# Optimization experiments

Measured on AMD Instinct MI355X. Metric: run time of the kernel, lower is better.

## Reference

```python
import jax, jax.numpy as jnp
import numpy as np

B, L, HID, NH = 4, 1024, 768, 12
HD = HID // NH  # head dim 64
VOCAB, MPE = 30, 2048
NW, WL = 8, 16
BETA = 1.0


def setup_inputs() -> dict:
    key = jax.random.key(0)
    ks = jax.random.split(key, 10)
    hidden_states = jax.random.normal(ks[0], (B, L, HID), dtype=jnp.float32)
    attention_mask = jnp.zeros((B, 1, 1, L), dtype=jnp.float32)
    distance = jax.random.randint(ks[1], (B, L, L), 0, 1022, dtype=jnp.int32)
    random_walk = jax.random.randint(ks[2], (B, L, NW, WL), 0, VOCAB, dtype=jnp.int32)
    anonymous_random_walk = jax.random.randint(ks[3], (B, L, NW, WL), 0, VOCAB, dtype=jnp.int32)
    s = 0.02
    Wq = jax.random.normal(ks[4], (HID, HID), dtype=jnp.float32) * s
    Wk = jax.random.normal(ks[5], (HID, HID), dtype=jnp.float32) * s
    Wv = jax.random.normal(ks[6], (HID, HID), dtype=jnp.float32) * s
    bq = jnp.zeros((HID,), jnp.float32)
    bk = jnp.zeros((HID,), jnp.float32)
    bv = jnp.zeros((HID,), jnp.float32)
    node_emb = jax.random.normal(ks[7], (VOCAB, HID), dtype=jnp.float32) * s
    node_emb = node_emb.at[0].set(0.0)  # padding_idx=0
    dist_emb = jax.random.normal(ks[8], (MPE, NH), dtype=jnp.float32) * s
    dist_emb = dist_emb.at[0].set(0.0)  # padding_idx=0
    return dict(hidden_states=hidden_states, attention_mask=attention_mask,
                Wq=Wq, bq=bq, Wk=Wk, bk=bk, Wv=Wv, bv=bv,
                node_emb=node_emb, dist_emb=dist_emb,
                distance=distance, random_walk=random_walk,
                anonymous_random_walk=anonymous_random_walk)


def _heads(x):  # [B,L,HID] -> [B,NH,L,HD]
    return x.reshape(B, L, NH, HD).transpose(0, 2, 1, 3)


def _walk_bias(walk, node_emb):
    # walk: [B,L,NW,WL] int -> embed [B,L,NW,WL,HID] -> sum dims (2,3) -> [B,L,HID]
    pe = jnp.sum(node_emb[walk], axis=(2, 3))
    e = _heads(pe)  # [B,NH,L,HD]
    return jnp.einsum('bhid,bhjd->bhij', e, e)


def reference(hidden_states, attention_mask, Wq, bq, Wk, bk, Wv, bv,
              node_emb, dist_emb, distance, random_walk, anonymous_random_walk):
    q = _heads(hidden_states @ Wq.T + bq)
    k = _heads(hidden_states @ Wk.T + bk)
    v = _heads(hidden_states @ Wv.T + bv)
    scores = jnp.einsum('bhid,bhjd->bhij', q, k) / np.sqrt(HD).astype(np.float32)
    # distance RPE: [B,L,L,NH] -> [B,NH,L,L]
    bias = dist_emb[distance + 1].transpose(0, 3, 1, 2)
    bias = bias + _walk_bias(random_walk, node_emb)
    bias = bias + _walk_bias(anonymous_random_walk, node_emb)
    scores = scores + bias * BETA + attention_mask
    probs = jax.nn.softmax(scores, axis=-1)
    ctx = jnp.einsum('bhij,bhjd->bhid', probs, v)
    return ctx.transpose(0, 2, 1, 3).reshape(B, L, HID)
```

## Files before the change

kernel.cpp:

```cpp
#include <hip/hip_runtime.h>
#include <hip/hip_bf16.h>

#define LL 1024
#define HID 768
#define NH 12
#define HD 64
#define KAUG 192
#define NBH 48

typedef unsigned int u32;
typedef unsigned short u16;
typedef __bf16 bf16_t;
typedef bf16_t bf16x8 __attribute__((ext_vector_type(8)));
typedef float f32x4 __attribute__((ext_vector_type(4)));
typedef u32 u32x4 __attribute__((ext_vector_type(4)));

__device__ __forceinline__ u16 f2b(float f) {
    union { float f; u32 u; } v; v.f = f;
    u32 r = v.u + 0x7fffu + ((v.u >> 16) & 1u);
    return (u16)(r >> 16);
}
__device__ __forceinline__ bf16x8 load8s(const u16* p) {
    return __builtin_bit_cast(bf16x8, *reinterpret_cast<const u32x4*>(p));
}
__device__ __forceinline__ void cvt4_store_v(u16* dst, float4 f) {
    ushort4 o;
    o.x = f2b(f.x); o.y = f2b(f.y); o.z = f2b(f.z); o.w = f2b(f.w);
    *reinterpret_cast<ushort4*>(dst) = o;
}

__global__ __launch_bounds__(256) void k_cvt(const float* __restrict__ hs,
                                             const float* __restrict__ Wq,
                                             const float* __restrict__ Wk,
                                             const float* __restrict__ Wv,
                                             u16* __restrict__ hs_b, u16* __restrict__ Wq_b,
                                             u16* __restrict__ Wk_b, u16* __restrict__ Wv_b) {
    int seg = blockIdx.y;
    const float* src = (seg == 0) ? hs : (seg == 1) ? Wq : (seg == 2) ? Wk : Wv;
    u16* dst         = (seg == 0) ? hs_b : (seg == 1) ? Wq_b : (seg == 2) ? Wk_b : Wv_b;
    int nchunk = (seg == 0) ? 786432 : 147456;
    int c = blockIdx.x * 256 + threadIdx.x;
    if (c >= nchunk) return;
    float4 f = *reinterpret_cast<const float4*>(&src[(size_t)c * 4]);
    cvt4_store_v(&dst[(size_t)c * 4], f);
}

__global__ __launch_bounds__(256) void k_qkv(const u16* __restrict__ hs_b,
                                             const u16* __restrict__ Wq_b, const u16* __restrict__ Wk_b,
                                             const u16* __restrict__ Wv_b,
                                             const float* __restrict__ bq, const float* __restrict__ bk,
                                             const float* __restrict__ bv,
                                             u16* __restrict__ Qa, u16* __restrict__ Ka,
                                             u16* __restrict__ Vt) {
    __shared__ __align__(16) u16 smem[18432];
    u16* a_s = smem;
    u16* b_s = smem + 9216;
    int m0 = blockIdx.x * 128;
    int nt = blockIdx.y;
    int which = nt / 6;
    int n0w = (nt % 6) * 128;
    const u16* W      = (which == 0) ? Wq_b : (which == 1) ? Wk_b : Wv_b;
    const float* bias = (which == 0) ? bq : (which == 1) ? bk : bv;
    int tid = threadIdx.x;
    int wave = tid >> 6, lane = tid & 63, l15 = lane & 15, qd = lane >> 4;
    int wm = wave >> 1, wn = wave & 1;

    f32x4 acc[4][4];
    for (int i = 0; i < 4; i++)
        for (int j = 0; j < 4; j++) acc[i][j] = f32x4{0.f, 0.f, 0.f, 0.f};

    u32x4 pa[4], pb[4];
#pragma unroll
    for (int it = 0; it < 4; it++) {
        int c = tid + it * 256;
        int row = c >> 3, col = (c & 7) * 8;
        pa[it] = *reinterpret_cast<const u32x4*>(&hs_b[(size_t)(m0 + row) * 768 + col]);
        pb[it] = *reinterpret_cast<const u32x4*>(&W[(size_t)(n0w + row) * 768 + col]);
    }
    for (int k0 = 0; k0 < 768; k0 += 64) {
        __syncthreads();
#pragma unroll
        for (int it = 0; it < 4; it++) {
            int c = tid + it * 256;
            int row = c >> 3, col = (c & 7) * 8;
            *reinterpret_cast<u32x4*>(&a_s[row * 72 + col]) = pa[it];
            *reinterpret_cast<u32x4*>(&b_s[row * 72 + col]) = pb[it];
        }
        __syncthreads();
        if (k0 < 704) {
            int k1 = k0 + 64;
#pragma unroll
            for (int it = 0; it < 4; it++) {
                int c = tid + it * 256;
                int row = c >> 3, col = (c & 7) * 8;
                pa[it] = *reinterpret_cast<const u32x4*>(&hs_b[(size_t)(m0 + row) * 768 + k1 + col]);
                pb[it] = *reinterpret_cast<const u32x4*>(&W[(size_t)(n0w + row) * 768 + k1 + col]);
            }
        }
        for (int kk = 0; kk < 2; kk++) {
            bf16x8 af[4], bf[4];
            for (int i = 0; i < 4; i++) af[i] = load8s(&a_s[(wm * 64 + i * 16 + l15) * 72 + kk * 32 + qd * 8]);
            for (int j = 0; j < 4; j++) bf[j] = load8s(&b_s[(wn * 64 + j * 16 + l15) * 72 + kk * 32 + qd * 8]);
            for (int i = 0; i < 4; i++)
                for (int j = 0; j < 4; j++)
                    acc[i][j] = __builtin_amdgcn_mfma_f32_16x16x32_bf16(af[i], bf[j], acc[i][j], 0, 0, 0);
        }
    }
    __syncthreads();
    int b = m0 >> 10, l0b = m0 & 1023;
    if (which != 2) {
        float qscale = (which == 0) ? 0.125f : 1.0f;
        for (int i = 0; i < 4; i++) {
            int m_loc = wm * 64 + i * 16 + qd * 4;
            for (int j = 0; j < 4; j++) {
                int n_loc = wn * 64 + j * 16 + l15;
                float bv_ = bias[n0w + n_loc];
                for (int r = 0; r < 4; r++)
                    smem[(m_loc + r) * 136 + n_loc] = f2b((acc[i][j][r] + bv_) * qscale);
            }
        }
        __syncthreads();
        u16* dstbuf = (which == 0) ? Qa : Ka;
        for (int it = 0; it < 8; it++) {
            int c = tid + it * 256;
            int row = c >> 4, col = (c & 15) * 8;
            u32x4 w = *reinterpret_cast<u32x4*>(&smem[row * 136 + col]);
            int nn = n0w + col;
            int h = nn >> 6, d = nn & 63;
            size_t dst = ((size_t)(b * NH + h) * LL + (l0b + row)) * KAUG + d;
            *reinterpret_cast<u32x4*>(&dstbuf[dst]) = w;
        }
    } else {
        for (int i = 0; i < 4; i++) {
            int m_loc = wm * 64 + i * 16 + qd * 4;
            for (int j = 0; j < 4; j++) {
                int n_loc = wn * 64 + j * 16 + l15;
                float bv_ = bias[n0w + n_loc];
                for (int r = 0; r < 4; r++)
                    smem[n_loc * 136 + (m_loc + r)] = f2b(acc[i][j][r] + bv_);
            }
        }
        __syncthreads();
        for (int it = 0; it < 8; it++) {
            int c = tid + it * 256;
            int n = c >> 4, m_off = (c & 15) * 8;
            u32x4 w = *reinterpret_cast<u32x4*>(&smem[n * 136 + m_off]);
            int nn = n0w + n;
            int h = nn >> 6, d = nn & 63;
            size_t dst = ((size_t)(b * NH + h) * HD + d) * LL + (l0b + m_off);
            *reinterpret_cast<u32x4*>(&Vt[dst]) = w;
        }
    }
}

__global__ __launch_bounds__(256) void k_pe(const int* __restrict__ rw,
                                            const int* __restrict__ arw,
                                            const float* __restrict__ node_emb,
                                            u16* __restrict__ Qa, u16* __restrict__ Ka) {
    int m = blockIdx.x;
    __shared__ int hist[64];
    __shared__ float c1[32], c2[32];
    int t = threadIdx.x;
    if (t < 64) hist[t] = 0;
    __syncthreads();
    if (t < 128) atomicAdd(&hist[rw[m * 128 + t] & 31], 1);
    else         atomicAdd(&hist[32 + (arw[m * 128 + (t - 128)] & 31)], 1);
    __syncthreads();
    if (t < 64) {
        if (t < 32) c1[t] = (float)hist[t];
        else        c2[t - 32] = (float)hist[t];
    }
    __syncthreads();
    int b = m >> 10, l = m & 1023;
    for (int c = t; c < 768; c += 256) {
        float s1 = 0.f, s2 = 0.f;
        for (int v = 0; v < 30; v++) {
            float ne = node_emb[v * 768 + c];
            s1 += c1[v] * ne;
            s2 += c2[v] * ne;
        }
        int h = c >> 6, d = c & 63;
        size_t base = ((size_t)(b * NH + h) * LL + l) * KAUG;
        u16 e1 = f2b(s1), e2 = f2b(s2);
        Qa[base + 64 + d] = e1;  Ka[base + 64 + d] = e1;
        Qa[base + 128 + d] = e2; Ka[base + 128 + d] = e2;
    }
}

__global__ __launch_bounds__(256) void k_attn(const u16* __restrict__ Qa, const u16* __restrict__ Ka,
                                              const u16* __restrict__ Vt,
                                              const int* __restrict__ distance,
                                              const float* __restrict__ dist_emb,
                                              const float* __restrict__ mask,
                                              void* __restrict__ outv, int f32mode) {
    __shared__ __align__(16) u16 ka_s[64][200];
    __shared__ __align__(16) u16 vt_s[64][72];
    __shared__ __align__(16) u16 p_s[4][16][72];

    int itile = blockIdx.x;
    int bh = blockIdx.y;
    int b = bh / NH, h = bh % NH;
    int tid = threadIdx.x, wave = tid >> 6, lane = tid & 63, l15 = lane & 15, qd = lane >> 4;

    const u16* Qh = Qa + (size_t)bh * LL * KAUG;
    const u16* Kh = Ka + (size_t)bh * LL * KAUG;
    const u16* Vh = Vt + (size_t)bh * HD * LL;
    const int* distb = distance + (size_t)b * LL * LL;
    const float* maskb = mask + (size_t)b * LL;
    const float* debh = dist_emb + h;

    int i0 = itile * 64 + wave * 16;
    bf16x8 aq[6];
    for (int ks = 0; ks < 6; ks++)
        aq[ks] = load8s(&Qh[(size_t)(i0 + l15) * KAUG + ks * 32 + qd * 8]);

    f32x4 o[4];
    for (int i = 0; i < 4; i++) o[i] = f32x4{0.f, 0.f, 0.f, 0.f};
    float m_i[4], l_i[4];
    for (int r = 0; r < 4; r++) { m_i[r] = -1e30f; l_i[r] = 0.f; }

    u32x4 kbuf[6], vbuf[2];
#pragma unroll
    for (int it = 0; it < 6; it++) {
        int c = tid + it * 256;
        int row = c / 24, col = (c % 24) * 8;
        kbuf[it] = *reinterpret_cast<const u32x4*>(&Kh[(size_t)row * KAUG + col]);
    }
#pragma unroll
    for (int it = 0; it < 2; it++) {
        int c = tid + it * 256;
        int d = c >> 3, col = (c & 7) * 8;
        vbuf[it] = *reinterpret_cast<const u32x4*>(&Vh[(size_t)d * LL + col]);
    }
    int dpre[16]; float mpre[4];
    for (int nf = 0; nf < 4; nf++) {
        int j_abs = nf * 16 + l15;
        mpre[nf] = maskb[j_abs];
        for (int r = 0; r < 4; r++)
            dpre[nf * 4 + r] = distb[(size_t)(i0 + qd * 4 + r) * LL + j_abs];
    }

    for (int jt = 0; jt < 16; jt++) {
        int j0 = jt * 64;
        __syncthreads();
#pragma unroll
        for (int it = 0; it < 6; it++) {
            int c = tid + it * 256;
            int row = c / 24, col = (c % 24) * 8;
            *reinterpret_cast<u32x4*>(&ka_s[row][col]) = kbuf[it];
        }
#pragma unroll
        for (int it = 0; it < 2; it++) {
            int c = tid + it * 256;
            int d = c >> 3, col = (c & 7) * 8;
            *reinterpret_cast<u32x4*>(&vt_s[d][col]) = vbuf[it];
        }
        __syncthreads();
        int dcur[16]; float mcur[4];
        for (int u_ = 0; u_ < 16; u_++) dcur[u_] = dpre[u_];
        for (int u_ = 0; u_ < 4; u_++)  mcur[u_] = mpre[u_];
        float bias_cur[16];
#pragma unroll
        for (int u_ = 0; u_ < 16; u_++)
            bias_cur[u_] = debh[(size_t)(dcur[u_] + 1) * NH];
        if (jt < 15) {
            int j0n = j0 + 64;
#pragma unroll
            for (int it = 0; it < 6; it++) {
                int c = tid + it * 256;
                int row = c / 24, col = (c % 24) * 8;
                kbuf[it] = *reinterpret_cast<const u32x4*>(&Kh[(size_t)(j0n + row) * KAUG + col]);
            }
#pragma unroll
            for (int it = 0; it < 2; it++) {
                int c = tid + it * 256;
                int d = c >> 3, col = (c & 7) * 8;
                vbuf[it] = *reinterpret_cast<const u32x4*>(&Vh[(size_t)d * LL + j0n + col]);
            }
            for (int nf = 0; nf < 4; nf++) {
                int j_abs = j0n + nf * 16 + l15;
                mpre[nf] = maskb[j_abs];
                for (int r = 0; r < 4; r++)
                    dpre[nf * 4 + r] = distb[(size_t)(i0 + qd * 4 + r) * LL + j_abs];
            }
        }

        f32x4 s[4];
        for (int nf = 0; nf < 4; nf++) {
            f32x4 accv = f32x4{0.f, 0.f, 0.f, 0.f};
            for (int ks = 0; ks < 6; ks++) {
                bf16x8 bfrag = load8s(&ka_s[nf * 16 + l15][ks * 32 + qd * 8]);
                accv = __builtin_amdgcn_mfma_f32_16x16x32_bf16(aq[ks], bfrag, accv, 0, 0, 0);
            }
            s[nf] = accv;
        }
        for (int nf = 0; nf < 4; nf++)
            for (int r = 0; r < 4; r++)
                s[nf][r] += bias_cur[nf * 4 + r] + mcur[nf];
        float mx[4];
        for (int r = 0; r < 4; r++) {
            float v = fmaxf(fmaxf(s[0][r], s[1][r]), fmaxf(s[2][r], s[3][r]));
            for (int off = 1; off < 16; off <<= 1) v = fmaxf(v, __shfl_xor(v, off));
            mx[r] = v;
        }
        float alpha[4], rs[4];
        for (int r = 0; r < 4; r++) {
            float mnew = fmaxf(m_i[r], mx[r]);
            alpha[r] = __expf(m_i[r] - mnew);
            m_i[r] = mnew;
            rs[r] = 0.f;
        }
        for (int nf = 0; nf < 4; nf++)
            for (int r = 0; r < 4; r++) {
                float p = __expf(s[nf][r] - m_i[r]);
                rs[r] += p;
                p_s[wave][qd * 4 + r][nf * 16 + l15] = f2b(p);
            }
        for (int r = 0; r < 4; r++) {
            float v = rs[r];
            for (int off = 1; off < 16; off <<= 1) v += __shfl_xor(v, off);
            l_i[r] = l_i[r] * alpha[r] + v;
        }
        for (int df = 0; df < 4; df++)
            for (int r = 0; r < 4; r++) o[df][r] *= alpha[r];
        __builtin_amdgcn_sched_barrier(0);
        asm volatile("" ::: "memory");
        for (int kstep = 0; kstep < 2; kstep++) {
            bf16x8 ap = load8s(&p_s[wave][l15][kstep * 32 + qd * 8]);
            for (int df = 0; df < 4; df++) {
                bf16x8 bv_ = load8s(&vt_s[df * 16 + l15][kstep * 32 + qd * 8]);
                o[df] = __builtin_amdgcn_mfma_f32_16x16x32_bf16(ap, bv_, o[df], 0, 0, 0);
            }
        }
    }
    for (int df = 0; df < 4; df++) {
        int d = df * 16 + l15;
        for (int r = 0; r < 4; r++) {
            int i_abs = i0 + qd * 4 + r;
            float v = o[df][r] / l_i[r];
            size_t idx = ((size_t)(b * LL) + i_abs) * HID + h * 64 + d;
            if (f32mode) ((float*)outv)[idx] = v;
            else         ((u16*)outv)[idx] = f2b(v);
        }
    }
}

extern "C" void kernel_launch(void* const* d_in, const int* in_sizes, int n_in,
                              void* d_out, int out_size, void* d_ws, size_t ws_size,
                              hipStream_t stream) {
    const float* hs       = (const float*)d_in[0];
    const float* mask     = (const float*)d_in[1];
    const float* Wq       = (const float*)d_in[2];
    const float* bq       = (const float*)d_in[3];
    const float* Wk       = (const float*)d_in[4];
    const float* bk       = (const float*)d_in[5];
    const float* Wv       = (const float*)d_in[6];
    const float* bv       = (const float*)d_in[7];
    const float* node_emb = (const float*)d_in[8];
    const float* dist_emb = (const float*)d_in[9];
    const int* distance   = (const int*)d_in[10];
    const int* rw         = (const int*)d_in[11];
    const int* arw        = (const int*)d_in[12];

    int f32mode = 0;
    {
        hipDeviceptr_t base = nullptr; size_t sz = 0;
        if (hipMemGetAddressRange(&base, &sz, (hipDeviceptr_t)d_out) == hipSuccess) {
            size_t off = (size_t)((char*)d_out - (char*)base);
            if (sz - off >= (size_t)out_size * 4u) f32mode = 1;
        }
    }

    u16* Qa   = (u16*)d_ws;
    u16* Ka   = Qa + (size_t)NBH * LL * KAUG;
    u16* Vt   = Ka + (size_t)NBH * LL * KAUG;
    u16* hs_b = Vt + (size_t)NBH * HD * LL;
    u16* Wq_b = hs_b + (size_t)4096 * 768;
    u16* Wk_b = Wq_b + (size_t)768 * 768;
    u16* Wv_b = Wk_b + (size_t)768 * 768;

    k_cvt<<<dim3(3072, 4), dim3(256), 0, stream>>>(hs, Wq, Wk, Wv, hs_b, Wq_b, Wk_b, Wv_b);
    k_qkv<<<dim3(32, 18), dim3(256), 0, stream>>>(hs_b, Wq_b, Wk_b, Wv_b, bq, bk, bv, Qa, Ka, Vt);
    k_pe<<<dim3(4096), dim3(256), 0, stream>>>(rw, arw, node_emb, Qa, Ka);
    k_attn<<<dim3(16, 48), dim3(256), 0, stream>>>(Qa, Ka, Vt, distance, dist_emb, mask, d_out, f32mode);
}
```

Baseline: 266.5 us.

## Stage per-head distance embedding in LDS, read V directly from global, raise occupancy

Each block now converts its head's column of dist_emb into a bf16 table in shared memory, so the per-element bias gather becomes an LDS lookup instead of a strided global load. The V tile is no longer staged through shared memory; MFMA B fragments are loaded straight from global/L2 memory. LDS padding is reduced and launch bounds request 4 blocks per SIMD to raise occupancy. The risks are extra global-load latency on the PV MFMA path, bf16 rounding of the distance bias, and register pressure from the occupancy hint.

```diff
diff --git a/kernel.cpp b/kernel.cpp
--- a/kernel.cpp
+++ b/kernel.cpp
@@ -19,6 +19,9 @@
     union { float f; u32 u; } v; v.f = f;
     u32 r = v.u + 0x7fffu + ((v.u >> 16) & 1u);
     return (u16)(r >> 16);
+}
+__device__ __forceinline__ float b2f(u16 u) {
+    union { u32 u; float f; } v; v.u = ((u32)u) << 16; return v.f;
 }
 __device__ __forceinline__ bf16x8 load8s(const u16* p) {
     return __builtin_bit_cast(bf16x8, *reinterpret_cast<const u32x4*>(p));
@@ -187,15 +190,15 @@
     }
 }
 
-__global__ __launch_bounds__(256) void k_attn(const u16* __restrict__ Qa, const u16* __restrict__ Ka,
-                                              const u16* __restrict__ Vt,
-                                              const int* __restrict__ distance,
-                                              const float* __restrict__ dist_emb,
-                                              const float* __restrict__ mask,
-                                              void* __restrict__ outv, int f32mode) {
-    __shared__ __align__(16) u16 ka_s[64][200];
-    __shared__ __align__(16) u16 vt_s[64][72];
-    __shared__ __align__(16) u16 p_s[4][16][72];
+__global__ __launch_bounds__(256, 4) void k_attn(const u16* __restrict__ Qa, const u16* __restrict__ Ka,
+                                                 const u16* __restrict__ Vt,
+                                                 const int* __restrict__ distance,
+                                                 const float* __restrict__ dist_emb,
+                                                 const float* __restrict__ mask,
+                                                 void* __restrict__ outv, int f32mode) {
+    __shared__ __align__(16) u16 ka_s[64][196];
+    __shared__ __align__(16) u16 p_s[4][16][68];
+    __shared__ u16 distcol[2048];
 
     int itile = blockIdx.x;
     int bh = blockIdx.y;
@@ -207,7 +210,8 @@
     const u16* Vh = Vt + (size_t)bh * HD * LL;
     const int* distb = distance + (size_t)b * LL * LL;
     const float* maskb = mask + (size_t)b * LL;
-    const float* debh = dist_emb + h;
+
+    for (int t = tid; t < 2048; t += 256) distcol[t] = f2b(dist_emb[t * NH + h]);
 
     int i0 = itile * 64 + wave * 16;
     bf16x8 aq[6];
@@ -219,18 +223,12 @@
     float m_i[4], l_i[4];
     for (int r = 0; r < 4; r++) { m_i[r] = -1e30f; l_i[r] = 0.f; }
 
-    u32x4 kbuf[6], vbuf[2];
+    u32x4 kbuf[6];
 #pragma unroll
     for (int it = 0; it < 6; it++) {
         int c = tid + it * 256;
         int row = c / 24, col = (c % 24) * 8;
         kbuf[it] = *reinterpret_cast<const u32x4*>(&Kh[(size_t)row * KAUG + col]);
-    }
-#pragma unroll
-    for (int it = 0; it < 2; it++) {
-        int c = tid + it * 256;
-        int d = c >> 3, col = (c & 7) * 8;
-        vbuf[it] = *reinterpret_cast<const u32x4*>(&Vh[(size_t)d * LL + col]);
     }
     int dpre[16]; float mpre[4];
     for (int nf = 0; nf < 4; nf++) {
@@ -249,20 +247,11 @@
             int row = c / 24, col = (c % 24) * 8;
             *reinterpret_cast<u32x4*>(&ka_s[row][col]) = kbuf[it];
         }
-#pragma unroll
-        for (int it = 0; it < 2; it++) {
-            int c = tid + it * 256;
-            int d = c >> 3, col = (c & 7) * 8;
-            *reinterpret_cast<u32x4*>(&vt_s[d][col]) = vbuf[it];
-        }
-        __syncthreads();
-        int dcur[16]; float mcur[4];
-        for (int u_ = 0; u_ < 16; u_++) dcur[u_] = dpre[u_];
-        for (int u_ = 0; u_ < 4; u_++)  mcur[u_] = mpre[u_];
+        __syncthreads();
         float bias_cur[16];
 #pragma unroll
         for (int u_ = 0; u_ < 16; u_++)
-            bias_cur[u_] = debh[(size_t)(dcur[u_] + 1) * NH];
+            bias_cur[u_] = b2f(distcol[dpre[u_] + 1]) + mpre[u_ >> 2];
         if (jt < 15) {
             int j0n = j0 + 64;
 #pragma unroll
@@ -270,12 +259,6 @@
                 int c = tid + it * 256;
                 int row = c / 24, col = (c % 24) * 8;
                 kbuf[it] = *reinterpret_cast<const u32x4*>(&Kh[(size_t)(j0n + row) * KAUG + col]);
-            }
-#pragma unroll
-            for (int it = 0; it < 2; it++) {
-                int c = tid + it * 256;
-                int d = c >> 3, col = (c & 7) * 8;
-                vbuf[it] = *reinterpret_cast<const u32x4*>(&Vh[(size_t)d * LL + j0n + col]);
             }
             for (int nf = 0; nf < 4; nf++) {
                 int j_abs = j0n + nf * 16 + l15;
@@ -296,7 +279,7 @@
         }
         for (int nf = 0; nf < 4; nf++)
             for (int r = 0; r < 4; r++)
-                s[nf][r] += bias_cur[nf * 4 + r] + mcur[nf];
+                s[nf][r] += bias_cur[nf * 4 + r];
         float mx[4];
         for (int r = 0; r < 4; r++) {
             float v = fmaxf(fmaxf(s[0][r], s[1][r]), fmaxf(s[2][r], s[3][r]));
@@ -328,7 +311,7 @@
         for (int kstep = 0; kstep < 2; kstep++) {
             bf16x8 ap = load8s(&p_s[wave][l15][kstep * 32 + qd * 8]);
             for (int df = 0; df < 4; df++) {
-                bf16x8 bv_ = load8s(&vt_s[df * 16 + l15][kstep * 32 + qd * 8]);
+                bf16x8 bv_ = load8s(&Vh[(size_t)(df * 16 + l15) * LL + j0 + kstep * 32 + qd * 8]);
                 o[df] = __builtin_amdgcn_mfma_f32_16x16x32_bf16(ap, bv_, o[df], 0, 0, 0);
             }
         }
```

New measurement: 358.6 us. 1.35x slower.
